# Performance work log

Hardware: AMD Instinct MI355X
Metric: run time of the kernel (lower is better)

Reference implementation:

```python
import jax, jax.numpy as jnp
import numpy as np

B, T, W, H, F = 256, 128, 32, 512, 1024


def setup_inputs() -> dict:
    key = jax.random.key(0)
    ks = jax.random.split(key, 8)
    s = 0.05
    return {
        "inputs": jax.random.normal(ks[0], (B, T, 2), jnp.float32),
        "Wk": jax.random.normal(ks[1], (2, 4 * H), jnp.float32) * s,
        "Wr": jax.random.normal(ks[2], (H, 4 * H), jnp.float32) * s,
        "b": jnp.zeros((4 * H,), jnp.float32),
        "Ww": jax.random.normal(ks[3], (H, 2), jnp.float32) * s,
        "bw": jnp.zeros((2,), jnp.float32),
        "Wc": jax.random.normal(ks[4], (2, H), jnp.float32) * s,
        "bc": jnp.zeros((H,), jnp.float32),
        "Wcc": jax.random.normal(ks[5], (W * H, F), jnp.float32) * s,
        "bcc": jnp.zeros((F,), jnp.float32),
        "Wp": jax.random.normal(ks[6], (F, 2), jnp.float32) * s,
        "bp": jnp.zeros((2,), jnp.float32),
        "Wco": jax.random.normal(ks[7], (F, 1), jnp.float32) * s,
        "bco": jnp.zeros((1,), jnp.float32),
    }


def _cell(x, h, c, Wk, Wr, b):
    # Keras LSTMCell: gate order i, f, g(candidate), o; sigmoid recurrent act, tanh act.
    z = x @ Wk + h @ Wr + b
    i, f, g, o = jnp.split(z, 4, axis=-1)
    c = jax.nn.sigmoid(f) * c + jax.nn.sigmoid(i) * jnp.tanh(g)
    h = jax.nn.sigmoid(o) * jnp.tanh(c)
    return h, c


def reference(inputs, Wk, Wr, b, Ww, bw, Wc, bc, Wcc, bcc, Wp, bp, Wco, bco):
    # Masking(-1.0) is a no-op for Gaussian inputs; dropout is identity at inference.
    warm_seq = jnp.swapaxes(inputs[:, W:], 0, 1)  # [T-W, B, 2]
    h0 = jnp.zeros((inputs.shape[0], H), inputs.dtype)
    c0 = jnp.zeros_like(h0)

    def warm_step(carry, x):
        h, c = carry
        h, c = _cell(x, h, c, Wk, Wr, b)
        return (h, c), None

    (h, c), _ = jax.lax.scan(warm_step, (h0, c0), warm_seq)
    warm_out = h  # warm_up_lstm_output, [B, H]
    pred0 = h @ Ww + bw  # dense_warm (linear activation), [B, 2]

    def dec_step(carry, _):
        h, c, pred = carry
        h, c = _cell(pred, h, c, Wk, Wr, b)
        pred = h @ Ww + bw
        return (h, c, pred), pred

    n_dec = T - W - 1  # range(1, time - warm_up_length)
    _, preds_rest = jax.lax.scan(dec_step, (h, c, pred0), None, length=n_dec)
    predictions = jnp.concatenate([pred0[None], preds_rest], axis=0)  # [T-W, B, 2]
    predictions = jnp.swapaxes(predictions, 0, 1)  # [B, T-W, 2]

    cand = jax.nn.relu(inputs[:, : W - 1] @ Wc + bc)  # [B, W-1, H]
    cand = cand.reshape(cand.shape[0], -1)  # flatten -> [B, (W-1)*H]
    cat = jnp.concatenate([warm_out, cand], axis=1)  # [B, W*H]
    ct = jax.nn.relu(cat @ Wcc + bcc)  # dense_concat, [B, F]
    candidate_prob = jax.nn.sigmoid(ct @ Wp + bp)  # [B, 2]
    candidate_cost = ct @ Wco + bco  # [B, 1]
    return predictions, candidate_cost, candidate_prob, inputs
```

## Files before the change

### kernel.cpp

```cpp
#include <hip/hip_runtime.h>
#include <hip/hip_bf16.h>
#include <stdint.h>

#define B_    256
#define T_    128
#define W_    32
#define H_    512
#define G4_   2048
#define TW_   96
#define STEPS_ 191
#define TEAMS 16
#define MEMBERS 16
#define ROWS  16
#define HC    32

typedef __attribute__((ext_vector_type(8))) short short8;
typedef __attribute__((ext_vector_type(4))) float f32x4;
typedef __attribute__((ext_vector_type(4))) uint32_t u32x4;

__device__ __forceinline__ unsigned short f2bf(float f) {
  uint32_t u = __float_as_uint(f);
  u += 0x7fffu + ((u >> 16) & 1u);
  return (unsigned short)(u >> 16);
}
__device__ __forceinline__ float sigm(float x) { return 1.f / (1.f + __expf(-x)); }
__device__ __forceinline__ float tanh_(float x) { return 1.f - 2.f / (1.f + __expf(2.f * x)); }

#define LOAD_CF(p)      __hip_atomic_load((p), __ATOMIC_RELAXED, __HIP_MEMORY_SCOPE_AGENT)
#define LOAD_CI(p)      __hip_atomic_load((p), __ATOMIC_RELAXED, __HIP_MEMORY_SCOPE_AGENT)
#define ARRIVE(p)       __hip_atomic_fetch_add((p), 1, __ATOMIC_RELAXED, __HIP_MEMORY_SCOPE_AGENT)

__device__ __forceinline__ u32x4 ld16c(const void* p) {
  u32x4 v;
  asm volatile("global_load_dwordx4 %0, %1, off sc0 sc1"
               : "=&v"(v) : "v"(p) : "memory");
  return v;
}
__device__ __forceinline__ void st16c(void* p, u32x4 v) {
  asm volatile("global_store_dwordx4 %0, %1, off sc0 sc1" :: "v"(p), "v"(v) : "memory");
}
__device__ __forceinline__ void stf16c(void* p, f32x4 v) {
  asm volatile("global_store_dwordx4 %0, %1, off sc0 sc1" :: "v"(p), "v"(v) : "memory");
}

#define GBT_RELU(C0, C1)                                                      \
  {                                                                           \
    const int kkl_ = gK - 512 + l4*8;                                         \
    const int hc_ = kkl_ & 511;                                               \
    const int wi_ = ((kkl_ >> 9) - gw0) * 2;                                  \
    {                                                                         \
      int row_ = bhalf*128 + (C0)*16 + l16;                                   \
      float x0_ = xin[row_][wi_], x1_ = xin[row_][wi_+1];                     \
      short8 bf_;                                                             \
      _Pragma("unroll")                                                       \
      for (int j = 0; j < 8; j++) {                                           \
        float v_ = fmaf(x0_, wc0[hc_+j], fmaf(x1_, wc1[hc_+j], bcl[hc_+j]));  \
        bf_[j] = (short)f2bf(fmaxf(v_, 0.f));                                 \
      }                                                                       \
      gacc[C0] = __builtin_amdgcn_mfma_f32_16x16x32_bf16(af, bf_, gacc[C0], 0,0,0); \
    }                                                                         \
    {                                                                         \
      int row_ = bhalf*128 + (C1)*16 + l16;                                   \
      float x0_ = xin[row_][wi_], x1_ = xin[row_][wi_+1];                     \
      short8 bf_;                                                             \
      _Pragma("unroll")                                                       \
      for (int j = 0; j < 8; j++) {                                           \
        float v_ = fmaf(x0_, wc0[hc_+j], fmaf(x1_, wc1[hc_+j], bcl[hc_+j]));  \
        bf_[j] = (short)f2bf(fmaxf(v_, 0.f));                                 \
      }                                                                       \
      gacc[C1] = __builtin_amdgcn_mfma_f32_16x16x32_bf16(af, bf_, gacc[C1], 0,0,0); \
    }                                                                         \
  }

#define GBT_WARM(C0, C1)                                                      \
  {                                                                           \
    const unsigned short* wb_ = warm + gK + l4*8;                             \
    u32x4 wv0_ = ld16c(wb_ + (size_t)(bhalf*128 + (C0)*16 + l16) * 512);      \
    u32x4 wv1_ = ld16c(wb_ + (size_t)(bhalf*128 + (C1)*16 + l16) * 512);      \
    asm volatile("s_waitcnt vmcnt(0)" ::: "memory");                          \
    __builtin_amdgcn_sched_barrier(0);                                        \
    short8 b0_ = *(const short8*)&wv0_;                                       \
    short8 b1_ = *(const short8*)&wv1_;                                       \
    gacc[C0] = __builtin_amdgcn_mfma_f32_16x16x32_bf16(af, b0_, gacc[C0], 0,0,0); \
    gacc[C1] = __builtin_amdgcn_mfma_f32_16x16x32_bf16(af, b1_, gacc[C1], 0,0,0); \
  }

__global__ __launch_bounds__(256, 1) void lstm_kernel(
    const float* __restrict__ inputs, const float* __restrict__ Wk,
    const float* __restrict__ Wr, const float* __restrict__ bias,
    const float* __restrict__ Ww, const float* __restrict__ bw,
    const float* __restrict__ Wc, const float* __restrict__ bc,
    const float* __restrict__ Wcc,
    unsigned short* __restrict__ h0buf, unsigned short* __restrict__ h1buf,
    float* __restrict__ pp0, float* __restrict__ pp1,
    unsigned short* __restrict__ warm, int* __restrict__ flags,
    float* __restrict__ partialT, float* __restrict__ out_pred)
{
  const int team = blockIdx.x & 15;
  const int member = blockIdx.x >> 4;
  const int rbase = team * ROWS;
  const int hbase = member * HC;
  const int tid = threadIdx.x;
  const int wave = tid >> 6;
  const int lane = tid & 63;
  const int l4 = lane >> 4, l16 = lane & 15;

  __shared__ unsigned short h_lds[ROWS][H_];
  __shared__ float x_all[TW_][ROWS][2];
  __shared__ float x_lds[ROWS][2];
  __shared__ float pp_lds[4][ROWS][2];
  __shared__ alignas(16) unsigned short h_out[ROWS][HC];
  __shared__ float wc0[512], wc1[512], bcl[512];
  __shared__ float xin[256][10];

  const int kc = blockIdx.x >> 5, gnc = blockIdx.x & 31;
  const bool iskc0 = (kc == 0);
  const int gw0 = iskc0 ? 0 : kc*4 - 1;

  for (int i = tid; i < TW_*ROWS*2; i += 256) {
    int tt = i >> 5, row = (i >> 1) & 15, c = i & 1;
    x_all[tt][row][c] = inputs[(size_t)(rbase+row)*(T_*2) + (W_+tt)*2 + c];
  }
  for (int i = tid; i < 512; i += 256) {
    wc0[i] = Wc[i]; wc1[i] = Wc[512 + i]; bcl[i] = bc[i];
  }
  for (int i = tid; i < 2560; i += 256) {
    int row = i / 10, r = i - row*10;
    xin[row][r] = inputs[(size_t)row*(T_*2) + gw0*2 + r];
  }

  const int gateL = l16 & 3, hclL = l16 >> 2;
  short8 afrag[2][16];
  float bbv[2][4], wk0v[2][4], wk1v[2][4], wwv[2][2];
#pragma unroll
  for (int a = 0; a < 2; a++) {
    const int gcA = gateL*H_ + hbase + wave*8 + a*4 + hclL;
#pragma unroll
    for (int ks = 0; ks < 16; ks++) {
      const float* wp = Wr + (size_t)(ks*32 + l4*8) * G4_ + gcA;
#pragma unroll
      for (int j = 0; j < 8; j++) afrag[a][ks][j] = (short)f2bf(wp[(size_t)j * G4_]);
    }
    const int colA = hbase + wave*8 + a*4 + l4;
#pragma unroll
    for (int j = 0; j < 4; j++) {
      int gcj = j*H_ + colA;
      bbv[a][j] = bias[gcj]; wk0v[a][j] = Wk[gcj]; wk1v[a][j] = Wk[G4_ + gcj];
    }
    wwv[a][0] = Ww[2*colA]; wwv[a][1] = Ww[2*colA + 1];
  }
  const float bwc0 = bw[0], bwc1 = bw[1];
  float creg[2] = {0.f, 0.f};

  auto KIDX = [&](int g) -> int {
    return iskc0 ? (g < 48 ? 512 + g*32 : (g - 48)*32) : kc*2048 + g*32;
  };
  const int nhalf = wave & 1, bhalf = wave >> 1;
  const int gnrow = gnc*32 + nhalf*16 + l16;
  f32x4 gacc[8];
#pragma unroll
  for (int i = 0; i < 8; i++) gacc[i] = (f32x4){0.f,0.f,0.f,0.f};
  short8 af;
  float fn[8];
  {
    const float* wp = Wcc + (size_t)(KIDX(0) + l4*8) * 1024 + gnrow;
#pragma unroll
    for (int j = 0; j < 8; j++) fn[j] = wp[(size_t)j * 1024];
  }
  int gq = -1, gK = 0, phase = 1;
  __syncthreads();

  int* ctr = flags + team * 16;
  int* gctr2 = flags + 256;
  const int srow = tid >> 4, sg = tid & 15;

  for (int t = 0; t < STEPS_; t++) {
    const unsigned short* hprev = (t & 1) ? h1buf : h0buf;
    unsigned short* hnext = (t & 1) ? h0buf : h1buf;
    const float* ppprev = (t & 1) ? pp1 : pp0;
    float* ppnext = (t & 1) ? pp0 : pp1;

    const bool dox = (t >= TW_) && (tid < 32);
    float vals[MEMBERS];
    if (dox) {
      int row = tid >> 1, c = tid & 1;
      const float* pps = ppprev + (size_t)team*MEMBERS*32 + row*2 + c;
#pragma unroll
      for (int m = 0; m < MEMBERS; m++) vals[m] = LOAD_CF(pps + m*32);
    }
    u32x4 q[4];
    {
      const unsigned short* srcb = hprev + (size_t)(rbase+srow)*H_ + sg*8;
#pragma unroll
      for (int i = 0; i < 4; i++) q[i] = ld16c(srcb + i*128);
    }
    if (gq >= 0 && gq < 64) {
      if (gK < 512) { if (!phase) GBT_WARM(0,1) else GBT_WARM(4,5) }
      else          { if (!phase) GBT_RELU(0,1) else GBT_RELU(4,5) }
    }
    asm volatile("s_waitcnt vmcnt(0)" ::: "memory");
    __builtin_amdgcn_sched_barrier(0);
#pragma unroll
    for (int i = 0; i < 4; i++)
      *(u32x4*)&h_lds[srow][((sg + 16*i) ^ (srow & 7)) * 8] = q[i];
    if (dox) {
      int row = tid >> 1, c = tid & 1;
      float s = c ? bwc1 : bwc0;
#pragma unroll
      for (int m = 0; m < MEMBERS; m++) s += vals[m];
      x_lds[row][c] = s;
      if (member == 0)
        out_pred[((size_t)(rbase+row)*96 + (t - TW_))*2 + c] = s;
    }
    __syncthreads();

    f32x4 acc[2];
    const float* xsrc = (t < TW_) ? &x_all[t][0][0] : &x_lds[0][0];
    {
      float x0 = xsrc[2*l16], x1 = xsrc[2*l16 + 1];
#pragma unroll
      for (int a = 0; a < 2; a++)
#pragma unroll
        for (int j = 0; j < 4; j++)
          acc[a][j] = bbv[a][j] + wk0v[a][j]*x0 + wk1v[a][j]*x1;
    }
#pragma unroll
    for (int ks = 0; ks < 16; ks++) {
      int pg = ((ks*4 + l4) ^ (l16 & 7)) * 8;
      short8 b0 = *(const short8*)&h_lds[l16][pg];
      acc[0] = __builtin_amdgcn_mfma_f32_16x16x32_bf16(afrag[0][ks], b0, acc[0], 0,0,0);
      acc[1] = __builtin_amdgcn_mfma_f32_16x16x32_bf16(afrag[1][ks], b0, acc[1], 0,0,0);
    }

    float pp0v = 0.f, pp1v = 0.f;
#pragma unroll
    for (int a = 0; a < 2; a++) {
      float zi = acc[a][0], zf = acc[a][1], zg = acc[a][2], zo = acc[a][3];
      float cn = sigm(zf)*creg[a] + sigm(zi)*tanh_(zg);
      float hn = sigm(zo)*tanh_(cn);
      creg[a] = cn;
      pp0v += hn * wwv[a][0];
      pp1v += hn * wwv[a][1];
      h_out[l16][wave*8 + a*4 + l4] = f2bf(hn);
    }
    if (t >= TW_ - 1) {
      pp0v += __shfl_xor(pp0v, 16); pp0v += __shfl_xor(pp0v, 32);
      pp1v += __shfl_xor(pp1v, 16); pp1v += __shfl_xor(pp1v, 32);
      if (l4 == 0) {
        pp_lds[wave][l16][0] = pp0v;
        pp_lds[wave][l16][1] = pp1v;
      }
    }
    __syncthreads();

    if (tid < 64) {
      int row = tid >> 2, qd = tid & 3;
      u32x4 v = *(const u32x4*)&h_out[row][qd*8];
      st16c(hnext + (size_t)(rbase+row)*H_ + hbase + qd*8, v);
      if (t == TW_ - 1)
        st16c(warm + (size_t)(rbase+row)*H_ + hbase + qd*8, v);
    }
    if (t >= TW_ - 1 && tid < 8) {
      f32x4 pv;
#pragma unroll
      for (int j = 0; j < 4; j++) {
        int idx = tid*4 + j, row = idx >> 1, c = idx & 1;
        pv[j] = pp_lds[0][row][c] + pp_lds[1][row][c]
              + pp_lds[2][row][c] + pp_lds[3][row][c];
      }
      stf16c(ppnext + (size_t)(team*MEMBERS + member)*32 + tid*4, pv);
    }

    asm volatile("s_waitcnt vmcnt(0)" ::: "memory");
    __syncthreads();
    if (tid == 0) {
      ARRIVE(ctr);
      if (t == TW_ - 1) ARRIVE(gctr2);
    }
    if (gq >= 0 && gq < 64) {
      if (gK < 512) { if (!phase) GBT_WARM(2,3) else GBT_WARM(6,7) }
      else          { if (!phase) GBT_RELU(2,3) else GBT_RELU(6,7) }
    }
    if (phase) {
      if (gq + 1 < 64) {
        gq++;
        gK = KIDX(gq);
#pragma unroll
        for (int j = 0; j < 8; j++) af[j] = (short)f2bf(fn[j]);
        if (iskc0 && gq == 48) {
          if (tid == 0) { while (LOAD_CI(gctr2) < 256) {} }
          __syncthreads();
        }
        if (gq + 1 < 64) {
          const float* wp = Wcc + (size_t)(KIDX(gq + 1) + l4*8) * 1024 + gnrow;
#pragma unroll
          for (int j = 0; j < 8; j++) fn[j] = wp[(size_t)j * 1024];
        }
      } else {
        gq = 64;
      }
    }
    phase ^= 1;
    if (tid == 0) {
      int need = MEMBERS * (t + 1);
      while (LOAD_CI(ctr) < need) {}
    }
    __syncthreads();
  }

  if (member == 0 && tid < 32) {
    int row = tid >> 1, c = tid & 1;
    const float* pps = pp1 + (size_t)team*MEMBERS*32 + row*2 + c;
    float s = c ? bwc1 : bwc0;
#pragma unroll
    for (int m = 0; m < MEMBERS; m++) s += LOAD_CF(pps + m*32);
    out_pred[((size_t)(rbase+row)*96 + 95)*2 + c] = s;
  }

  {
    float* pp = partialT + (size_t)kc*262144
              + (size_t)(gnc*32 + nhalf*16 + l4*4)*256 + bhalf*128 + l16;
#pragma unroll
    for (int bt = 0; bt < 8; bt++)
#pragma unroll
      for (int r = 0; r < 4; r++)
        pp[(size_t)r*256 + bt*16] = gacc[bt][r];
  }
}

__global__ void reduce_kernel(const float* __restrict__ partialT,
                              const float* __restrict__ bcc, float* __restrict__ ctT,
                              const float* __restrict__ inputs, float* __restrict__ out)
{
  int e = blockIdx.x * 256 + threadIdx.x;
  int n = e >> 8;
  float s = bcc[n];
#pragma unroll
  for (int p = 0; p < 8; p++) s += partialT[(size_t)p*262144 + e];
  ctT[e] = fmaxf(s, 0.f);
  if (e < 65536) out[49920 + e] = inputs[e];
}

__global__ void head_kernel(const float* __restrict__ ctT, const float* __restrict__ Wp,
                            const float* __restrict__ bp, const float* __restrict__ Wco,
                            const float* __restrict__ bco, float* __restrict__ out)
{
  int b = blockIdx.x;
  int lane = threadIdx.x;
  float p0 = 0.f, p1 = 0.f, pc = 0.f;
#pragma unroll
  for (int i = 0; i < 16; i++) {
    int n = i*64 + lane;
    float c = ctT[(size_t)n*256 + b];
    p0 += c * Wp[2*n]; p1 += c * Wp[2*n+1]; pc += c * Wco[n];
  }
  for (int m = 1; m < 64; m <<= 1) {
    p0 += __shfl_xor(p0, m); p1 += __shfl_xor(p1, m); pc += __shfl_xor(pc, m);
  }
  if (lane == 0) {
    out[49152 + b]       = pc + bco[0];
    out[49408 + 2*b]     = 1.f / (1.f + __expf(-(p0 + bp[0])));
    out[49408 + 2*b + 1] = 1.f / (1.f + __expf(-(p1 + bp[1])));
  }
}

extern "C" void kernel_launch(void* const* d_in, const int* in_sizes, int n_in,
                              void* d_out, int out_size, void* d_ws, size_t ws_size,
                              hipStream_t stream) {
  const float* inputs = (const float*)d_in[0];
  const float* Wk   = (const float*)d_in[1];
  const float* Wr   = (const float*)d_in[2];
  const float* bias = (const float*)d_in[3];
  const float* Ww   = (const float*)d_in[4];
  const float* bw   = (const float*)d_in[5];
  const float* Wc   = (const float*)d_in[6];
  const float* bc   = (const float*)d_in[7];
  const float* Wcc  = (const float*)d_in[8];
  const float* bcc  = (const float*)d_in[9];
  const float* Wp   = (const float*)d_in[10];
  const float* bp   = (const float*)d_in[11];
  const float* Wco  = (const float*)d_in[12];
  const float* bco  = (const float*)d_in[13];
  float* out = (float*)d_out;
  char* ws = (char*)d_ws;

  unsigned short* h0   = (unsigned short*)(ws);
  int*            flags= (int*)(ws + 0x40000);
  unsigned short* h1   = (unsigned short*)(ws + 0x42000);
  unsigned short* warm = (unsigned short*)(ws + 0x82000);
  float*          pp0  = (float*)(ws + 0xC2000);
  float*          pp1  = (float*)(ws + 0xCA000);
  float*          partialT = (float*)(ws + 0x8C2000);
  float*          ctT  = (float*)(ws + 0x10C2000);

  hipMemsetAsync(d_ws, 0, 0x42000, stream);

  lstm_kernel<<<TEAMS*MEMBERS, 256, 0, stream>>>(inputs, Wk, Wr, bias, Ww, bw,
                                                 Wc, bc, Wcc,
                                                 h0, h1, pp0, pp1, warm, flags,
                                                 partialT, out);
  reduce_kernel<<<1024, 256, 0, stream>>>(partialT, bcc, ctT, inputs, out);
  head_kernel<<<256, 64, 0, stream>>>(ctT, Wp, bp, Wco, bco, out);
}
```

Baseline: 634.2 us.

## Precompute ReLU candidate features to global bf16 buffer before recurrent loop

Before the LSTM loop, the blocks sharing a K-chunk cooperatively compute the ReLU(x@Wc+bc) candidate activations once, pack them to bf16 and store them in a global workspace. They then synchronize through a per-chunk counter. Inside the loop, the interleaved dense_concat MFMA slices load these precomputed operands instead of recomputing FMAs and bf16 conversions on every step. This removes redundant ALU work from the latency-critical recurrent loop and frees the xin LDS array, at the cost of a prologue pass, extra global memory traffic and a spin barrier.

Result: slower. 681.4 us (+7.4%).

```diff
diff --git a/kernel.cpp b/kernel.cpp
--- a/kernel.cpp
+++ b/kernel.cpp
@@ -43,33 +43,17 @@
   asm volatile("global_store_dwordx4 %0, %1, off sc0 sc1" :: "v"(p), "v"(v) : "memory");
 }
 
-#define GBT_RELU(C0, C1)                                                      \
+#define GBT_CAT(C0, C1)                                                       \
   {                                                                           \
-    const int kkl_ = gK - 512 + l4*8;                                         \
-    const int hc_ = kkl_ & 511;                                               \
-    const int wi_ = ((kkl_ >> 9) - gw0) * 2;                                  \
-    {                                                                         \
-      int row_ = bhalf*128 + (C0)*16 + l16;                                   \
-      float x0_ = xin[row_][wi_], x1_ = xin[row_][wi_+1];                     \
-      short8 bf_;                                                             \
-      _Pragma("unroll")                                                       \
-      for (int j = 0; j < 8; j++) {                                           \
-        float v_ = fmaf(x0_, wc0[hc_+j], fmaf(x1_, wc1[hc_+j], bcl[hc_+j]));  \
-        bf_[j] = (short)f2bf(fmaxf(v_, 0.f));                                 \
-      }                                                                       \
-      gacc[C0] = __builtin_amdgcn_mfma_f32_16x16x32_bf16(af, bf_, gacc[C0], 0,0,0); \
-    }                                                                         \
-    {                                                                         \
-      int row_ = bhalf*128 + (C1)*16 + l16;                                   \
-      float x0_ = xin[row_][wi_], x1_ = xin[row_][wi_+1];                     \
-      short8 bf_;                                                             \
-      _Pragma("unroll")                                                       \
-      for (int j = 0; j < 8; j++) {                                           \
-        float v_ = fmaf(x0_, wc0[hc_+j], fmaf(x1_, wc1[hc_+j], bcl[hc_+j]));  \
-        bf_[j] = (short)f2bf(fmaxf(v_, 0.f));                                 \
-      }                                                                       \
-      gacc[C1] = __builtin_amdgcn_mfma_f32_16x16x32_bf16(af, bf_, gacc[C1], 0,0,0); \
-    }                                                                         \
+    const unsigned short* cb_ = catg + (size_t)kc*524288 + gq*32 + l4*8;      \
+    u32x4 v0_ = ld16c(cb_ + (size_t)(bhalf*128 + (C0)*16 + l16) * 2048);      \
+    u32x4 v1_ = ld16c(cb_ + (size_t)(bhalf*128 + (C1)*16 + l16) * 2048);      \
+    asm volatile("s_waitcnt vmcnt(0)" ::: "memory");                          \
+    __builtin_amdgcn_sched_barrier(0);                                        \
+    short8 b0_ = *(const short8*)&v0_;                                        \
+    short8 b1_ = *(const short8*)&v1_;                                        \
+    gacc[C0] = __builtin_amdgcn_mfma_f32_16x16x32_bf16(af, b0_, gacc[C0], 0,0,0); \
+    gacc[C1] = __builtin_amdgcn_mfma_f32_16x16x32_bf16(af, b1_, gacc[C1], 0,0,0); \
   }
 
 #define GBT_WARM(C0, C1)                                                      \
@@ -93,7 +77,8 @@
     const float* __restrict__ Wcc,
     unsigned short* __restrict__ h0buf, unsigned short* __restrict__ h1buf,
     float* __restrict__ pp0, float* __restrict__ pp1,
-    unsigned short* __restrict__ warm, int* __restrict__ flags,
+    unsigned short* __restrict__ warm, unsigned short* __restrict__ catg,
+    int* __restrict__ flags,
     float* __restrict__ partialT, float* __restrict__ out_pred)
 {
   const int team = blockIdx.x & 15;
@@ -111,11 +96,10 @@
   __shared__ float pp_lds[4][ROWS][2];
   __shared__ alignas(16) unsigned short h_out[ROWS][HC];
   __shared__ float wc0[512], wc1[512], bcl[512];
-  __shared__ float xin[256][10];
 
   const int kc = blockIdx.x >> 5, gnc = blockIdx.x & 31;
   const bool iskc0 = (kc == 0);
-  const int gw0 = iskc0 ? 0 : kc*4 - 1;
+  const int nks = iskc0 ? 48 : 64;
 
   for (int i = tid; i < TW_*ROWS*2; i += 256) {
     int tt = i >> 5, row = (i >> 1) & 15, c = i & 1;
@@ -124,10 +108,6 @@
   for (int i = tid; i < 512; i += 256) {
     wc0[i] = Wc[i]; wc1[i] = Wc[512 + i]; bcl[i] = bc[i];
   }
-  for (int i = tid; i < 2560; i += 256) {
-    int row = i / 10, r = i - row*10;
-    xin[row][r] = inputs[(size_t)row*(T_*2) + gw0*2 + r];
-  }
 
   const int gateL = l16 & 3, hclL = l16 >> 2;
   short8 afrag[2][16];
@@ -151,6 +131,45 @@
   }
   const float bwc0 = bw[0], bwc1 = bw[1];
   float creg[2] = {0.f, 0.f};
+  __syncthreads();
+
+  int* ctr = flags + team * 16;
+  int* gctr2 = flags + 256;
+  int* catctr = flags + 512 + kc * 16;
+
+  {
+    const int r0 = gnc * 8;
+    const int ngr = nks * 4;
+    for (int i = tid; i < 8 * ngr; i += 256) {
+      int rl = i / ngr, g16 = i - rl * ngr;
+      int row = r0 + rl;
+      int col = g16 * 8;
+      int kg = iskc0 ? 512 + col : kc*2048 + col;
+      int kkf = kg - 512;
+      int w = kkf >> 9, hc = kkf & 511;
+      float x0 = inputs[(size_t)row*(T_*2) + w*2];
+      float x1 = inputs[(size_t)row*(T_*2) + w*2 + 1];
+      unsigned short v8[8];
+#pragma unroll
+      for (int j = 0; j < 8; j++) {
+        float v = fmaf(x0, wc0[hc+j], fmaf(x1, wc1[hc+j], bcl[hc+j]));
+        v8[j] = f2bf(fmaxf(v, 0.f));
+      }
+      u32x4 pk;
+      pk.x = (uint32_t)v8[0] | ((uint32_t)v8[1] << 16);
+      pk.y = (uint32_t)v8[2] | ((uint32_t)v8[3] << 16);
+      pk.z = (uint32_t)v8[4] | ((uint32_t)v8[5] << 16);
+      pk.w = (uint32_t)v8[6] | ((uint32_t)v8[7] << 16);
+      st16c(catg + ((size_t)kc*256 + row)*2048 + col, pk);
+    }
+    asm volatile("s_waitcnt vmcnt(0)" ::: "memory");
+    __syncthreads();
+    if (tid == 0) {
+      ARRIVE(catctr);
+      while (LOAD_CI(catctr) < 32) {}
+    }
+    __syncthreads();
+  }
 
   auto KIDX = [&](int g) -> int {
     return iskc0 ? (g < 48 ? 512 + g*32 : (g - 48)*32) : kc*2048 + g*32;
@@ -168,10 +187,7 @@
     for (int j = 0; j < 8; j++) fn[j] = wp[(size_t)j * 1024];
   }
   int gq = -1, gK = 0, phase = 1;
-  __syncthreads();
-
-  int* ctr = flags + team * 16;
-  int* gctr2 = flags + 256;
+
   const int srow = tid >> 4, sg = tid & 15;
 
   for (int t = 0; t < STEPS_; t++) {
@@ -196,7 +212,7 @@
     }
     if (gq >= 0 && gq < 64) {
       if (gK < 512) { if (!phase) GBT_WARM(0,1) else GBT_WARM(4,5) }
-      else          { if (!phase) GBT_RELU(0,1) else GBT_RELU(4,5) }
+      else          { if (!phase) GBT_CAT(0,1)  else GBT_CAT(4,5) }
     }
     asm volatile("s_waitcnt vmcnt(0)" ::: "memory");
     __builtin_amdgcn_sched_barrier(0);
@@ -279,7 +295,7 @@
     }
     if (gq >= 0 && gq < 64) {
       if (gK < 512) { if (!phase) GBT_WARM(2,3) else GBT_WARM(6,7) }
-      else          { if (!phase) GBT_RELU(2,3) else GBT_RELU(6,7) }
+      else          { if (!phase) GBT_CAT(2,3)  else GBT_CAT(6,7) }
     }
     if (phase) {
       if (gq + 1 < 64) {
@@ -390,15 +406,16 @@
   unsigned short* warm = (unsigned short*)(ws + 0x82000);
   float*          pp0  = (float*)(ws + 0xC2000);
   float*          pp1  = (float*)(ws + 0xCA000);
-  float*          partialT = (float*)(ws + 0x8C2000);
-  float*          ctT  = (float*)(ws + 0x10C2000);
+  unsigned short* catg = (unsigned short*)(ws + 0xD2000);
+  float*          partialT = (float*)(ws + 0x8D2000);
+  float*          ctT  = (float*)(ws + 0x10D2000);
 
   hipMemsetAsync(d_ws, 0, 0x42000, stream);
 
   lstm_kernel<<<TEAMS*MEMBERS, 256, 0, stream>>>(inputs, Wk, Wr, bias, Ww, bw,
                                                  Wc, bc, Wcc,
-                                                 h0, h1, pp0, pp1, warm, flags,
-                                                 partialT, out);
+                                                 h0, h1, pp0, pp1, warm, catg,
+                                                 flags, partialT, out);
   reduce_kernel<<<1024, 256, 0, stream>>>(partialT, bcc, ctT, inputs, out);
   head_kernel<<<256, 64, 0, stream>>>(ctT, Wp, bp, Wco, bco, out);
 }
```
